# Kernel tuning notes

Measured on AMD Instinct MI355X. Metric: run time of the kernel, lower is better.

## Reference

```python
import jax, jax.numpy as jnp
import numpy as np

H, F, D, E, L = 8, 768, 128, 256, 13   # heads, feat_dim, compression_dim, embed_dim, nb_layer
B, T = 8, 1000
DCOR = D * (D - 1) // 2                # 8128, upper-triangle (offset=1) correlation features


def setup_inputs() -> dict:
    key = jax.random.key(0)
    ks = jax.random.split(key, 12)
    s = lambda k, shape, sc=0.02: jax.random.normal(k, shape, jnp.float32) * sc
    return {
        "x": jax.random.normal(ks[0], (B, F, T, L), jnp.float32),
        "weights_k": jnp.ones((H, L), jnp.float32),
        "weights_v": jnp.ones((H, L), jnp.float32),
        "q": jax.random.normal(ks[1], (H, D), jnp.float32),
        "Wk": s(ks[2], (H, D, F)), "bk": s(ks[3], (H, D)),
        "Wv": s(ks[4], (H, D, F)), "bv": s(ks[5], (H, D)),
        "Wproj": s(ks[6], (H, E, DCOR)), "bproj": s(ks[7], (H, E)),
        "WT": s(ks[8], (E, H * D)), "bT": s(ks[9], (E,)),
        "Wp": s(ks[10], (E, H * E)), "bp": s(ks[11], (E,)),
    }


def _norm_t(z):
    # normalize over the time axis; torch .var() is unbiased (ddof=1)
    mu = z.mean(axis=2, keepdims=True)
    sd = jnp.sqrt(z.var(axis=2, keepdims=True, ddof=1)) + 1e-9
    return (z - mu) / sd


def _forward(x, weights_k, weights_v, q, Wk, bk, Wv, bv, Wproj, bproj, WT, bT, Wp, bp):
    # x: [B, F, T, L]; per-head softmax-weighted layer sum -> [B, H, T, F]
    kw = jax.nn.softmax(weights_k, axis=-1)  # [H, L]
    vw = jax.nn.softmax(weights_v, axis=-1)
    k_raw = jnp.einsum('bftl,hl->bhtf', x, kw)
    v_raw = jnp.einsum('bftl,hl->bhtf', x, vw)
    # per-head compression linears -> [B, H, T, D]
    mh_k = jnp.einsum('bhtf,hdf->bhtd', k_raw, Wk) + bk[None, :, None, :]
    mh_v = jnp.einsum('bhtf,hdf->bhtd', v_raw, Wv) + bv[None, :, None, :]
    # single-query scaled-dot-product attention pooling per head
    scores = jnp.einsum('hd,bhtd->bht', q, mh_k) / jnp.sqrt(jnp.float32(D))
    attn = jax.nn.softmax(scores, axis=-1)
    o1 = jnp.einsum('bht,bhtd->bhd', attn, mh_v)           # [B, H, D]
    out_T = o1.reshape(B, H * D) @ WT.T + bT               # [B, E]
    # correlation branch (mh_q = mh_v): time-normalize, D x D correlation, triu(offset=1)
    k_n = _norm_t(mh_k)
    q_n = _norm_t(mh_v)
    corr = jnp.einsum('bhtk,bhtl->bhkl', k_n, q_n) / T     # [B, H, D, D]
    iu0, iu1 = np.triu_indices(D, k=1)
    mh_corr = corr[:, :, iu0, iu1]                         # [B, H, DCOR]
    outs = jnp.einsum('bhc,hec->bhe', mh_corr, Wproj) + bproj[None]
    out_F = outs.reshape(B, H * E) @ Wp.T + bp             # [B, E]
    return 0.5 * out_F + 0.5 * out_T


def reference(x, weights_k, weights_v, q, Wk, bk, Wv, bv, Wproj, bproj, WT, bT, Wp, bp):
    return _forward(x, weights_k, weights_v, q, Wk, bk, Wv, bv, Wproj, bproj, WT, bT, Wp, bp)
```

## Files before the change

### kernel.cpp

```cpp
#include <hip/hip_runtime.h>
#include <hip/hip_bf16.h>

#define Hn 8
#define Fn 768
#define Dn 128
#define En 256
#define Ln 13
#define Bn 8
#define Tn 1000
#define TPn 1024
#define NCOR 8128

typedef float f32x4 __attribute__((ext_vector_type(4)));
typedef __bf16 bf16x8 __attribute__((ext_vector_type(8)));
typedef unsigned short u16;

static __device__ __forceinline__ u16 f2bf(float f) {
  __hip_bfloat16 h = __float2bfloat16(f);
  return __builtin_bit_cast(u16, h);
}
static __device__ __forceinline__ float bf2f(u16 u) {
  return __bfloat162float(__builtin_bit_cast(__hip_bfloat16, u));
}

static __device__ __forceinline__ void gload_lds16(const u16* g, u16* lds_wave_base) {
  __builtin_amdgcn_global_load_lds(
      (const __attribute__((address_space(1))) unsigned int*)g,
      (__attribute__((address_space(3))) unsigned int*)lds_wave_base, 16, 0, 0);
}

__global__ __launch_bounds__(256) void k1_raw(
    const float* __restrict__ x,
    const float* __restrict__ wk, const float* __restrict__ wv,
    const float* __restrict__ Wk, const float* __restrict__ Wv,
    u16* __restrict__ kv_raw, u16* __restrict__ Wbf,
    float* __restrict__ s1, float* __restrict__ s2,
    int b0, int BG) {
  __shared__ float kvw[16 * Ln];
  __shared__ u16 res[16 * 32 * 34];
  int tid = threadIdx.x;
  if (tid < 16) {
    int kvi = tid >> 3, h = tid & 7;
    const float* w = (kvi ? wv : wk) + h * Ln;
    float m = -1e30f;
    for (int l = 0; l < Ln; ++l) m = fmaxf(m, w[l]);
    float e[Ln], s = 0.f;
    for (int l = 0; l < Ln; ++l) { e[l] = expf(w[l] - m); s += e[l]; }
    for (int l = 0; l < Ln; ++l) kvw[tid * Ln + l] = e[l] / s;
  }
  if (b0 == 0) {
    int nb = gridDim.x * gridDim.y * gridDim.z;
    int lin = blockIdx.x + gridDim.x * (blockIdx.y + gridDim.y * blockIdx.z);
    int n = 2 * Hn * Dn * Fn;
    for (int i = lin * 256 + tid; i < n; i += nb * 256) {
      float v = (i < Hn * Dn * Fn) ? Wk[i] : Wv[i - Hn * Dn * Fn];
      Wbf[i] = f2bf(v);
    }
    int ns = 2 * Bn * Hn * Dn;
    for (int i = lin * 256 + tid; i < ns; i += nb * 256) { s1[i] = 0.f; s2[i] = 0.f; }
  }
  int t0 = blockIdx.x * 32, f0 = blockIdx.y * 32;
  int b_l = blockIdx.z, b = b0 + b_l;
  int fl = tid & 31, tq = tid >> 5;
  int tbase = t0 + tq * 4;
  bool valid = (tbase < Tn);
  float4 xq[13];
  if (valid) {
    const float4* xp = (const float4*)(x + ((size_t)(b * Fn + f0 + fl) * Tn + tbase) * Ln);
#pragma unroll
    for (int i = 0; i < 13; ++i) xq[i] = xp[i];
  }
  __syncthreads();
  const float* xf = (const float*)xq;
  for (int o = 0; o < 16; ++o) {
    float a0 = 0.f, a1 = 0.f, a2 = 0.f, a3 = 0.f;
    if (valid) {
#pragma unroll
      for (int l = 0; l < Ln; ++l) {
        float w = kvw[o * Ln + l];
        a0 += xf[l] * w;
        a1 += xf[Ln + l] * w;
        a2 += xf[2 * Ln + l] * w;
        a3 += xf[3 * Ln + l] * w;
      }
    }
    int rb = o * 1088 + tq * 4 * 34 + fl;
    res[rb] = f2bf(a0);
    res[rb + 34] = f2bf(a1);
    res[rb + 68] = f2bf(a2);
    res[rb + 102] = f2bf(a3);
  }
  __syncthreads();
  int part = tid & 3;
#pragma unroll
  for (int it = 0; it < 8; ++it) {
    int r = (tid >> 2) + it * 64;
    int o = r >> 5, tl = r & 31;
    int kv = o >> 3, h = o & 7;
    const u16* src = res + o * 1088 + tl * 34 + part * 8;
    uint4 v;
    v.x = *(const unsigned*)(src + 0);
    v.y = *(const unsigned*)(src + 2);
    v.z = *(const unsigned*)(src + 4);
    v.w = *(const unsigned*)(src + 6);
    u16* dst = kv_raw + (((size_t)(kv * BG + b_l) * Hn + h) * TPn + t0 + tl) * Fn + f0 + part * 8;
    *reinterpret_cast<uint4*>(dst) = v;
  }
}

__global__ __launch_bounds__(256) void k2_gemm(
    const u16* __restrict__ kv_raw, const u16* __restrict__ Wbf,
    const float* __restrict__ bk, const float* __restrict__ bv,
    const float* __restrict__ qg,
    u16* __restrict__ mhT, float* __restrict__ s1buf, float* __restrict__ s2buf,
    float* __restrict__ scores, int b0, int BG) {
  __shared__ __align__(16) char ldsbuf[33280];
  __shared__ float qsh[Dn];
  u16* As0 = (u16*)ldsbuf;
  u16* Bs0 = (u16*)(ldsbuf + 8192);
  u16* As1 = (u16*)(ldsbuf + 16384);
  u16* Bs1 = (u16*)(ldsbuf + 24576);
  u16* Cst = (u16*)ldsbuf;
  int tid = threadIdx.x, lane = tid & 63, w = tid >> 6;
  int t0 = blockIdx.x * 128;
  int b_l = blockIdx.y / Hn, h = blockIdx.y % Hn, kv = blockIdx.z;
  int b = b0 + b_l;
  if (tid < Dn) qsh[tid] = qg[h * Dn + tid];
  const u16* Abase = kv_raw + ((size_t)(kv * BG + b_l) * Hn + h) * TPn * Fn + (size_t)t0 * Fn;
  const u16* Bbase = Wbf + ((size_t)(kv * Hn + h)) * Dn * Fn;
  f32x4 acc[4][4];
#pragma unroll
  for (int mi = 0; mi < 4; ++mi)
#pragma unroll
    for (int ni = 0; ni < 4; ++ni) acc[mi][ni] = (f32x4){0.f, 0.f, 0.f, 0.f};
  int wm = (w >> 1) * 64, wn = (w & 1) * 64;
  int lin0 = tid, lin1 = tid + 256;
  int row0 = lin0 >> 2, part0 = lin0 & 3;
  int row1 = lin1 >> 2, part1 = lin1 & 3;
  int wb0 = (w * 64) * 8, wb1 = (256 + w * 64) * 8;

  auto STAGE = [&](int f0, u16* Ad, u16* Bd) {
    gload_lds16(Abase + (size_t)row0 * Fn + f0 + part0 * 8, Ad + wb0);
    gload_lds16(Abase + (size_t)row1 * Fn + f0 + part1 * 8, Ad + wb1);
    gload_lds16(Bbase + (size_t)row0 * Fn + f0 + part0 * 8, Bd + wb0);
    gload_lds16(Bbase + (size_t)row1 * Fn + f0 + part1 * 8, Bd + wb1);
  };
  auto COMPUTE = [&](const u16* Ac, const u16* Bc) {
    bf16x8 af[4], bg[4];
#pragma unroll
    for (int mi = 0; mi < 4; ++mi)
      af[mi] = *(const bf16x8*)(Ac + (wm + mi * 16 + (lane & 15)) * 32 + (lane >> 4) * 8);
#pragma unroll
    for (int ni = 0; ni < 4; ++ni)
      bg[ni] = *(const bf16x8*)(Bc + (wn + ni * 16 + (lane & 15)) * 32 + (lane >> 4) * 8);
#pragma unroll
    for (int mi = 0; mi < 4; ++mi)
#pragma unroll
      for (int ni = 0; ni < 4; ++ni)
        acc[mi][ni] = __builtin_amdgcn_mfma_f32_16x16x32_bf16(af[mi], bg[ni], acc[mi][ni], 0, 0, 0);
  };

  STAGE(0, As0, Bs0);
  __syncthreads();
  for (int f0 = 0; f0 < Fn; f0 += 64) {
    if (f0 + 32 < Fn) STAGE(f0 + 32, As1, Bs1);
    COMPUTE(As0, Bs0);
    __syncthreads();
    if (f0 + 64 < Fn) STAGE(f0 + 64, As0, Bs0);
    COMPUTE(As1, Bs1);
    __syncthreads();
  }

  float bias[4];
  const float* bptr = (kv ? bv : bk) + h * Dn;
#pragma unroll
  for (int ni = 0; ni < 4; ++ni) bias[ni] = bptr[wn + ni * 16 + (lane & 15)];
#pragma unroll
  for (int mi = 0; mi < 4; ++mi)
#pragma unroll
    for (int ni = 0; ni < 4; ++ni)
#pragma unroll
      for (int r = 0; r < 4; ++r) {
        int row = wm + mi * 16 + (lane >> 4) * 4 + r;
        int col = wn + ni * 16 + (lane & 15);
        float v = acc[mi][ni][r] + bias[ni];
        if (t0 + row >= Tn) v = 0.f;
        Cst[row * 130 + col] = f2bf(v);
      }
  __syncthreads();
  int d = tid >> 1, half = tid & 1;
  u16* orow = mhT + (((size_t)(kv * Bn + b) * Hn + h) * Dn + d) * TPn + t0;
  float ssum = 0.f, ssq = 0.f;
#pragma unroll
  for (int j = 0; j < 8; ++j) {
    int tb = half * 64 + j * 8;
    u16 pk[8];
#pragma unroll
    for (int ii = 0; ii < 8; ++ii) {
      u16 ub = Cst[(tb + ii) * 130 + d];
      pk[ii] = ub;
      float vr = bf2f(ub);
      ssum += vr;
      ssq += vr * vr;
    }
    uint4 v4;
    v4.x = (unsigned)pk[0] | ((unsigned)pk[1] << 16);
    v4.y = (unsigned)pk[2] | ((unsigned)pk[3] << 16);
    v4.z = (unsigned)pk[4] | ((unsigned)pk[5] << 16);
    v4.w = (unsigned)pk[6] | ((unsigned)pk[7] << 16);
    *reinterpret_cast<uint4*>(orow + tb) = v4;
  }
  int sidx = ((kv * Bn + b) * Hn + h) * Dn + d;
  atomicAdd(&s1buf[sidx], ssum);
  atomicAdd(&s2buf[sidx], ssq);

  if (kv == 0) {
    int t = tid >> 1, hf = tid & 1;
    float s = 0.f;
    const u16* crow = Cst + t * 130 + hf * 64;
    const float* qh = qsh + hf * 64;
#pragma unroll
    for (int dd = 0; dd < 64; ++dd) s += qh[dd] * bf2f(crow[dd]);
    s += __shfl_xor(s, 1);
    if (hf == 0)
      scores[((size_t)b * Hn + h) * TPn + t0 + t] =
          (t0 + t < Tn) ? s * 0.088388347648318447f : -1e30f;
  }
}

__global__ __launch_bounds__(256) void k34(
    const u16* __restrict__ mhT, const float* __restrict__ scores,
    const float* __restrict__ s1buf, const float* __restrict__ s2buf,
    float* __restrict__ o1, float* __restrict__ corr) {
  __shared__ float sc[TPn];
  __shared__ float red[256];
  __shared__ __align__(16) u16 Kt0[1024], Vt0[4096], Kt1[1024], Vt1[4096];
  __shared__ float mkS[32], skS[32], mvS[128], svS[128];
  int tid = threadIdx.x;
  int lane = tid & 63, w = tid >> 6;
  if (blockIdx.x < 256) {
    int bh = blockIdx.x >> 2, dq = blockIdx.x & 3;
    int b = bh >> 3, h = bh & 7;
    const float* srow = scores + (size_t)bh * TPn;
    float4 z4 = *((const float4*)srow + tid);
    float z[4] = {z4.x, z4.y, z4.z, z4.w};
    float m = fmaxf(fmaxf(z[0], z[1]), fmaxf(z[2], z[3]));
#pragma unroll
    for (int off = 32; off; off >>= 1) m = fmaxf(m, __shfl_xor(m, off));
    if (lane == 0) red[w] = m;
    __syncthreads();
    m = fmaxf(fmaxf(red[0], red[1]), fmaxf(red[2], red[3]));
    float lsum = 0.f;
#pragma unroll
    for (int j = 0; j < 4; ++j) {
      float e = __expf(z[j] - m);
      sc[tid * 4 + j] = e;
      lsum += e;
    }
#pragma unroll
    for (int off = 32; off; off >>= 1) lsum += __shfl_xor(lsum, off);
    if (lane == 0) red[4 + w] = lsum;
    __syncthreads();
    float inv = 1.f / (red[4] + red[5] + red[6] + red[7]);
    int dl = tid & 31, slice = tid >> 5;
    int d = dq * 32 + dl;
    const u16* Vr = mhT + ((size_t)(1 * Bn + b) * Hn + h) * Dn * TPn + (size_t)d * TPn + slice * 128;
    const float* at = sc + slice * 128;
    float a = 0.f;
#pragma unroll
    for (int i = 0; i < 16; ++i) {
      bf16x8 vv = *(const bf16x8*)(Vr + i * 8);
#pragma unroll
      for (int j = 0; j < 8; ++j) a += at[i * 8 + j] * (float)vv[j];
    }
    a += __shfl_xor(a, 32);
    __syncthreads();
    if (lane < 32) red[w * 32 + dl] = a;
    __syncthreads();
    if (tid < 32)
      o1[((size_t)b * Hn + h) * Dn + dq * 32 + tid] =
          inv * (red[tid] + red[32 + tid] + red[64 + tid] + red[96 + tid]);
    return;
  }
  int id = blockIdx.x - 256;
  int bh = id & 63, rq = id >> 6;
  int b = bh >> 3, h = bh & 7;
  const u16* Kb = mhT + ((size_t)(0 * Bn + b) * Hn + h) * Dn * TPn + (size_t)(rq * 32) * TPn;
  const u16* Vb = mhT + ((size_t)(1 * Bn + b) * Hn + h) * Dn * TPn;
  if (tid < 32) {
    int dd = rq * 32 + tid;
    int sidx = ((0 * Bn + b) * Hn + h) * Dn + dd;
    float a1 = s1buf[sidx], a2 = s2buf[sidx];
    float mu = a1 / (float)Tn;
    float var = (a2 - a1 * a1 / (float)Tn) / (float)(Tn - 1);
    mkS[tid] = mu;
    skS[tid] = sqrtf(fmaxf(var, 0.f)) + 1e-9f;
  } else if (tid < 160) {
    int dd = tid - 32;
    int sidx = ((1 * Bn + b) * Hn + h) * Dn + dd;
    float a1 = s1buf[sidx], a2 = s2buf[sidx];
    float mu = a1 / (float)Tn;
    float var = (a2 - a1 * a1 / (float)Tn) / (float)(Tn - 1);
    mvS[dd] = mu;
    svS[dd] = sqrtf(fmaxf(var, 0.f)) + 1e-9f;
  }
  f32x4 acc[2][2];
#pragma unroll
  for (int mi = 0; mi < 2; ++mi)
#pragma unroll
    for (int ni = 0; ni < 2; ++ni) acc[mi][ni] = (f32x4){0.f, 0.f, 0.f, 0.f};
  int rowK = tid >> 2, partK = tid & 3;
  int wbK = (w * 64) * 8;
  int rowV0 = tid >> 2, partV0 = tid & 3;
  int rowV1 = (tid + 256) >> 2, partV1 = tid & 3;
  int wbV0 = (w * 64) * 8, wbV1 = (256 + w * 64) * 8;

  auto STAGE = [&](int t0, u16* Kd, u16* Vd) {
    if (w < 2)
      gload_lds16(Kb + (size_t)rowK * TPn + t0 + partK * 8, Kd + wbK);
    gload_lds16(Vb + (size_t)rowV0 * TPn + t0 + partV0 * 8, Vd + wbV0);
    gload_lds16(Vb + (size_t)rowV1 * TPn + t0 + partV1 * 8, Vd + wbV1);
  };
  auto COMPUTE = [&](const u16* Kc, const u16* Vc) {
    bf16x8 af[2], bg[2];
#pragma unroll
    for (int mi = 0; mi < 2; ++mi)
      af[mi] = *(const bf16x8*)(Kc + (mi * 16 + (lane & 15)) * 32 + (lane >> 4) * 8);
#pragma unroll
    for (int ni = 0; ni < 2; ++ni)
      bg[ni] = *(const bf16x8*)(Vc + (w * 32 + ni * 16 + (lane & 15)) * 32 + (lane >> 4) * 8);
#pragma unroll
    for (int mi = 0; mi < 2; ++mi)
#pragma unroll
      for (int ni = 0; ni < 2; ++ni)
        acc[mi][ni] = __builtin_amdgcn_mfma_f32_16x16x32_bf16(af[mi], bg[ni], acc[mi][ni], 0, 0, 0);
  };

  STAGE(0, Kt0, Vt0);
  __syncthreads();
  for (int s = 0; s < TPn; s += 64) {
    if (s + 32 < TPn) STAGE(s + 32, Kt1, Vt1);
    COMPUTE(Kt0, Vt0);
    __syncthreads();
    if (s + 64 < TPn) STAGE(s + 64, Kt0, Vt0);
    COMPUTE(Kt1, Vt1);
    __syncthreads();
  }
  const float invT = 1.f / (float)Tn;
#pragma unroll
  for (int mi = 0; mi < 2; ++mi)
#pragma unroll
    for (int ni = 0; ni < 2; ++ni)
#pragma unroll
      for (int r = 0; r < 4; ++r) {
        int ml = mi * 16 + (lane >> 4) * 4 + r;
        int nn = w * 32 + ni * 16 + (lane & 15);
        int mm = rq * 32 + ml;
        if (nn > mm) {
          float S = acc[mi][ni][r];
          float cv = (S - (float)Tn * mkS[ml] * mvS[nn]) * invT / (skS[ml] * svS[nn]);
          int cidx = mm * (2 * Dn - mm - 1) / 2 + (nn - mm - 1);
          corr[(size_t)bh * NCOR + cidx] = cv;
        }
      }
}

__global__ __launch_bounds__(256) void k5_proj(
    const float* __restrict__ corr, const float* __restrict__ Wproj,
    const float* __restrict__ bproj, float* __restrict__ outs) {
  __shared__ float red[8 * 256];
  int tid = threadIdx.x;
  int e = blockIdx.x, h = blockIdx.y;
  const float4* wp4 = (const float4*)(Wproj + ((size_t)h * En + e) * NCOR);
  float accs[8];
#pragma unroll
  for (int b = 0; b < 8; ++b) accs[b] = 0.f;
  for (int k = 0; k < 8; ++k) {
    int c4 = tid + k * 256;
    if (c4 < NCOR / 4) {
      float4 wv = wp4[c4];
#pragma unroll
      for (int b = 0; b < 8; ++b) {
        float4 cv = *((const float4*)(corr + ((size_t)b * Hn + h) * NCOR) + c4);
        accs[b] += wv.x * cv.x + wv.y * cv.y + wv.z * cv.z + wv.w * cv.w;
      }
    }
  }
#pragma unroll
  for (int b = 0; b < 8; ++b) red[b * 256 + tid] = accs[b];
  __syncthreads();
  for (int s = 128; s > 0; s >>= 1) {
    if (tid < s) {
#pragma unroll
      for (int b = 0; b < 8; ++b) red[b * 256 + tid] += red[b * 256 + tid + s];
    }
    __syncthreads();
  }
  if (tid < 8) outs[((size_t)tid * Hn + h) * En + e] = red[tid * 256] + bproj[h * En + e];
}

__global__ __launch_bounds__(256) void k5_final(
    const float* __restrict__ outs, const float* __restrict__ o1,
    const float* __restrict__ WT, const float* __restrict__ bT,
    const float* __restrict__ Wp, const float* __restrict__ bp,
    float* __restrict__ out) {
  __shared__ float os[2048];
  __shared__ float o1s[1024];
  __shared__ float redF[256], redT[256];
  int tid = threadIdx.x;
  int b = blockIdx.x >> 3, ic = blockIdx.x & 7;
  for (int i = tid; i < 2048; i += 256) os[i] = outs[(size_t)b * 2048 + i];
  for (int i = tid; i < 1024; i += 256) o1s[i] = o1[(size_t)b * 1024 + i];
  __syncthreads();
  int il = tid >> 3, slice = tid & 7;
  int i = ic * 32 + il;
  const float* wpr = Wp + (size_t)i * 2048;
  const float* wtr = WT + (size_t)i * 1024;
  float aF = 0.f, aT = 0.f;
  for (int kk = 0; kk < 256; ++kk) { int j = kk * 8 + slice; aF += os[j] * wpr[j]; }
  for (int kk = 0; kk < 128; ++kk) { int j = kk * 8 + slice; aT += o1s[j] * wtr[j]; }
  redF[tid] = aF; redT[tid] = aT;
  __syncthreads();
  for (int s = 4; s > 0; s >>= 1) {
    if (slice < s) { redF[tid] += redF[tid + s]; redT[tid] += redT[tid + s]; }
    __syncthreads();
  }
  if (slice == 0) {
    float oF = redF[tid] + bp[i];
    float oT = redT[tid] + bT[i];
    out[(size_t)b * En + i] = 0.5f * oF + 0.5f * oT;
  }
}

extern "C" void kernel_launch(void* const* d_in, const int* in_sizes, int n_in,
                              void* d_out, int out_size, void* d_ws, size_t ws_size,
                              hipStream_t stream) {
  const float* x     = (const float*)d_in[0];
  const float* wk    = (const float*)d_in[1];
  const float* wv    = (const float*)d_in[2];
  const float* q     = (const float*)d_in[3];
  const float* Wk    = (const float*)d_in[4];
  const float* bk    = (const float*)d_in[5];
  const float* Wv    = (const float*)d_in[6];
  const float* bv    = (const float*)d_in[7];
  const float* Wproj = (const float*)d_in[8];
  const float* bproj = (const float*)d_in[9];
  const float* WT    = (const float*)d_in[10];
  const float* bT    = (const float*)d_in[11];
  const float* Wp    = (const float*)d_in[12];
  const float* bp    = (const float*)d_in[13];
  float* out = (float*)d_out;

  char* ws = (char*)d_ws;
  size_t off = 0;
  auto alloc = [&](size_t bytes) { size_t p = off; off += (bytes + 255) & ~(size_t)255; return p; };
  u16*   Wbf    = (u16*)  (ws + alloc((size_t)2 * Hn * Dn * Fn * 2));
  u16*   mhT    = (u16*)  (ws + alloc((size_t)2 * Bn * Hn * Dn * TPn * 2));
  float* s1     = (float*)(ws + alloc((size_t)2 * Bn * Hn * Dn * 4));
  float* s2     = (float*)(ws + alloc((size_t)2 * Bn * Hn * Dn * 4));
  float* o1     = (float*)(ws + alloc((size_t)Bn * Hn * Dn * 4));
  float* corr   = (float*)(ws + alloc((size_t)Bn * Hn * NCOR * 4));
  float* outs   = (float*)(ws + alloc((size_t)Bn * Hn * En * 4));
  float* scores = (float*)(ws + alloc((size_t)Bn * Hn * TPn * 4));
  size_t fixed = off;
  size_t per_b = (size_t)2 * Hn * TPn * Fn * 2;
  int BG = 8;
  while (BG > 1 && fixed + (size_t)BG * per_b > ws_size) BG >>= 1;
  u16* kv_raw = (u16*)(ws + fixed);

  for (int b0 = 0; b0 < Bn; b0 += BG) {
    k1_raw<<<dim3(32, 24, BG), 256, 0, stream>>>(x, wk, wv, Wk, Wv, kv_raw, Wbf, s1, s2, b0, BG);
    k2_gemm<<<dim3(8, Hn * BG, 2), 256, 0, stream>>>(kv_raw, Wbf, bk, bv, q, mhT, s1, s2,
                                                     scores, b0, BG);
  }
  k34<<<512, 256, 0, stream>>>(mhT, scores, s1, s2, o1, corr);
  k5_proj<<<dim3(En, Hn), 256, 0, stream>>>(corr, Wproj, bproj, outs);
  k5_final<<<64, 256, 0, stream>>>(outs, o1, WT, bT, Wp, bp, out);
}
```

Before: 661.0 us.

## Retile correlation and projection kernels, reorder GEMM grid, use nontemporal x loads

The correlation kernel now has each block compute 64 K-rows instead of 32, which halves the number of correlation blocks and the re-reads of the V tiles. The projection kernel now computes 8 output features per block, so each loaded corr vector is reused across 8 Wproj rows, and the shared-memory tree reduction is replaced by wave shuffles. The k2 grid is reordered so batch-head varies fastest. The one-shot x reads use nontemporal loads. The trade-off is higher register pressure (64 accumulators in the projection kernel) and fewer blocks, which may lower occupancy.

```diff
diff --git a/kernel.cpp b/kernel.cpp
--- a/kernel.cpp
+++ b/kernel.cpp
@@ -64,11 +64,11 @@
   int fl = tid & 31, tq = tid >> 5;
   int tbase = t0 + tq * 4;
   bool valid = (tbase < Tn);
-  float4 xq[13];
+  f32x4 xq[13];
   if (valid) {
-    const float4* xp = (const float4*)(x + ((size_t)(b * Fn + f0 + fl) * Tn + tbase) * Ln);
-#pragma unroll
-    for (int i = 0; i < 13; ++i) xq[i] = xp[i];
+    const f32x4* xp = (const f32x4*)(x + ((size_t)(b * Fn + f0 + fl) * Tn + tbase) * Ln);
+#pragma unroll
+    for (int i = 0; i < 13; ++i) xq[i] = __builtin_nontemporal_load(xp + i);
   }
   __syncthreads();
   const float* xf = (const float*)xq;
@@ -122,8 +122,10 @@
   u16* Bs1 = (u16*)(ldsbuf + 24576);
   u16* Cst = (u16*)ldsbuf;
   int tid = threadIdx.x, lane = tid & 63, w = tid >> 6;
-  int t0 = blockIdx.x * 128;
-  int b_l = blockIdx.y / Hn, h = blockIdx.y % Hn, kv = blockIdx.z;
+  int bh_lin = blockIdx.x;
+  int b_l = bh_lin / Hn, h = bh_lin % Hn;
+  int t0 = blockIdx.y * 128;
+  int kv = blockIdx.z;
   int b = b0 + b_l;
   if (tid < Dn) qsh[tid] = qg[h * Dn + tid];
   const u16* Abase = kv_raw + ((size_t)(kv * BG + b_l) * Hn + h) * TPn * Fn + (size_t)t0 * Fn;
@@ -234,12 +236,13 @@
     float* __restrict__ o1, float* __restrict__ corr) {
   __shared__ float sc[TPn];
   __shared__ float red[256];
-  __shared__ __align__(16) u16 Kt0[1024], Vt0[4096], Kt1[1024], Vt1[4096];
-  __shared__ float mkS[32], skS[32], mvS[128], svS[128];
+  __shared__ __align__(16) u16 Kt0[4096 / 2], Vt0[4096], Kt1[4096 / 2], Vt1[4096];
+  __shared__ float mkS[64], skS[64], mvS[128], svS[128];
   int tid = threadIdx.x;
   int lane = tid & 63, w = tid >> 6;
-  if (blockIdx.x < 256) {
-    int bh = blockIdx.x >> 2, dq = blockIdx.x & 3;
+  if (blockIdx.x >= 128) {
+    int id = blockIdx.x - 128;
+    int bh = id >> 2, dq = id & 3;
     int b = bh >> 3, h = bh & 7;
     const float* srow = scores + (size_t)bh * TPn;
     float4 z4 = *((const float4*)srow + tid);
@@ -282,21 +285,21 @@
           inv * (red[tid] + red[32 + tid] + red[64 + tid] + red[96 + tid]);
     return;
   }
-  int id = blockIdx.x - 256;
-  int bh = id & 63, rq = id >> 6;
+  int id = blockIdx.x;
+  int bh = id & 63, rh = id >> 6;
   int b = bh >> 3, h = bh & 7;
-  const u16* Kb = mhT + ((size_t)(0 * Bn + b) * Hn + h) * Dn * TPn + (size_t)(rq * 32) * TPn;
+  const u16* Kb = mhT + ((size_t)(0 * Bn + b) * Hn + h) * Dn * TPn + (size_t)(rh * 64) * TPn;
   const u16* Vb = mhT + ((size_t)(1 * Bn + b) * Hn + h) * Dn * TPn;
-  if (tid < 32) {
-    int dd = rq * 32 + tid;
+  if (tid < 64) {
+    int dd = rh * 64 + tid;
     int sidx = ((0 * Bn + b) * Hn + h) * Dn + dd;
     float a1 = s1buf[sidx], a2 = s2buf[sidx];
     float mu = a1 / (float)Tn;
     float var = (a2 - a1 * a1 / (float)Tn) / (float)(Tn - 1);
     mkS[tid] = mu;
     skS[tid] = sqrtf(fmaxf(var, 0.f)) + 1e-9f;
-  } else if (tid < 160) {
-    int dd = tid - 32;
+  } else if (tid < 192) {
+    int dd = tid - 64;
     int sidx = ((1 * Bn + b) * Hn + h) * Dn + dd;
     float a1 = s1buf[sidx], a2 = s2buf[sidx];
     float mu = a1 / (float)Tn;
@@ -304,33 +307,31 @@
     mvS[dd] = mu;
     svS[dd] = sqrtf(fmaxf(var, 0.f)) + 1e-9f;
   }
-  f32x4 acc[2][2];
-#pragma unroll
-  for (int mi = 0; mi < 2; ++mi)
+  f32x4 acc[4][2];
+#pragma unroll
+  for (int mi = 0; mi < 4; ++mi)
 #pragma unroll
     for (int ni = 0; ni < 2; ++ni) acc[mi][ni] = (f32x4){0.f, 0.f, 0.f, 0.f};
-  int rowK = tid >> 2, partK = tid & 3;
-  int wbK = (w * 64) * 8;
-  int rowV0 = tid >> 2, partV0 = tid & 3;
-  int rowV1 = (tid + 256) >> 2, partV1 = tid & 3;
-  int wbV0 = (w * 64) * 8, wbV1 = (256 + w * 64) * 8;
+  int rowA = tid >> 2, partA = tid & 3;
+  int rowV1 = 64 + (tid >> 2);
+  int wbA = (w * 64) * 8;
+  int wbV1 = 2048 + (w * 64) * 8;
 
   auto STAGE = [&](int t0, u16* Kd, u16* Vd) {
-    if (w < 2)
-      gload_lds16(Kb + (size_t)rowK * TPn + t0 + partK * 8, Kd + wbK);
-    gload_lds16(Vb + (size_t)rowV0 * TPn + t0 + partV0 * 8, Vd + wbV0);
-    gload_lds16(Vb + (size_t)rowV1 * TPn + t0 + partV1 * 8, Vd + wbV1);
+    gload_lds16(Kb + (size_t)rowA * TPn + t0 + partA * 8, Kd + wbA);
+    gload_lds16(Vb + (size_t)rowA * TPn + t0 + partA * 8, Vd + wbA);
+    gload_lds16(Vb + (size_t)rowV1 * TPn + t0 + partA * 8, Vd + wbV1);
   };
   auto COMPUTE = [&](const u16* Kc, const u16* Vc) {
-    bf16x8 af[2], bg[2];
-#pragma unroll
-    for (int mi = 0; mi < 2; ++mi)
+    bf16x8 af[4], bg[2];
+#pragma unroll
+    for (int mi = 0; mi < 4; ++mi)
       af[mi] = *(const bf16x8*)(Kc + (mi * 16 + (lane & 15)) * 32 + (lane >> 4) * 8);
 #pragma unroll
     for (int ni = 0; ni < 2; ++ni)
       bg[ni] = *(const bf16x8*)(Vc + (w * 32 + ni * 16 + (lane & 15)) * 32 + (lane >> 4) * 8);
 #pragma unroll
-    for (int mi = 0; mi < 2; ++mi)
+    for (int mi = 0; mi < 4; ++mi)
 #pragma unroll
       for (int ni = 0; ni < 2; ++ni)
         acc[mi][ni] = __builtin_amdgcn_mfma_f32_16x16x32_bf16(af[mi], bg[ni], acc[mi][ni], 0, 0, 0);
@@ -348,14 +349,14 @@
   }
   const float invT = 1.f / (float)Tn;
 #pragma unroll
-  for (int mi = 0; mi < 2; ++mi)
+  for (int mi = 0; mi < 4; ++mi)
 #pragma unroll
     for (int ni = 0; ni < 2; ++ni)
 #pragma unroll
       for (int r = 0; r < 4; ++r) {
         int ml = mi * 16 + (lane >> 4) * 4 + r;
         int nn = w * 32 + ni * 16 + (lane & 15);
-        int mm = rq * 32 + ml;
+        int mm = rh * 64 + ml;
         if (nn > mm) {
           float S = acc[mi][ni][r];
           float cv = (S - (float)Tn * mkS[ml] * mvS[nn]) * invT / (skS[ml] * svS[nn]);
@@ -368,35 +369,44 @@
 __global__ __launch_bounds__(256) void k5_proj(
     const float* __restrict__ corr, const float* __restrict__ Wproj,
     const float* __restrict__ bproj, float* __restrict__ outs) {
-  __shared__ float red[8 * 256];
-  int tid = threadIdx.x;
-  int e = blockIdx.x, h = blockIdx.y;
-  const float4* wp4 = (const float4*)(Wproj + ((size_t)h * En + e) * NCOR);
-  float accs[8];
-#pragma unroll
-  for (int b = 0; b < 8; ++b) accs[b] = 0.f;
+  __shared__ float red[256];
+  int tid = threadIdx.x, lane = tid & 63, w = tid >> 6;
+  int h = blockIdx.x & 7, ec = blockIdx.x >> 3;
+  float acc[8][8];
+#pragma unroll
+  for (int ei = 0; ei < 8; ++ei)
+#pragma unroll
+    for (int b = 0; b < 8; ++b) acc[ei][b] = 0.f;
   for (int k = 0; k < 8; ++k) {
     int c4 = tid + k * 256;
     if (c4 < NCOR / 4) {
-      float4 wv = wp4[c4];
-#pragma unroll
-      for (int b = 0; b < 8; ++b) {
-        float4 cv = *((const float4*)(corr + ((size_t)b * Hn + h) * NCOR) + c4);
-        accs[b] += wv.x * cv.x + wv.y * cv.y + wv.z * cv.z + wv.w * cv.w;
+      float4 cv[8];
+#pragma unroll
+      for (int b = 0; b < 8; ++b)
+        cv[b] = *((const float4*)(corr + ((size_t)b * Hn + h) * NCOR) + c4);
+#pragma unroll
+      for (int ei = 0; ei < 8; ++ei) {
+        float4 wv = *((const float4*)(Wproj + ((size_t)h * En + ec * 8 + ei) * NCOR) + c4);
+#pragma unroll
+        for (int b = 0; b < 8; ++b)
+          acc[ei][b] += wv.x * cv[b].x + wv.y * cv[b].y + wv.z * cv[b].z + wv.w * cv[b].w;
       }
     }
   }
-#pragma unroll
-  for (int b = 0; b < 8; ++b) red[b * 256 + tid] = accs[b];
-  __syncthreads();
-  for (int s = 128; s > 0; s >>= 1) {
-    if (tid < s) {
-#pragma unroll
-      for (int b = 0; b < 8; ++b) red[b * 256 + tid] += red[b * 256 + tid + s];
-    }
-    __syncthreads();
-  }
-  if (tid < 8) outs[((size_t)tid * Hn + h) * En + e] = red[tid * 256] + bproj[h * En + e];
+  const float* af = &acc[0][0];
+#pragma unroll
+  for (int v = 0; v < 64; ++v) {
+    float s = af[v];
+#pragma unroll
+    for (int off = 32; off; off >>= 1) s += __shfl_xor(s, off);
+    if (lane == 0) red[w * 64 + v] = s;
+  }
+  __syncthreads();
+  if (tid < 64) {
+    int ei = tid >> 3, b = tid & 7;
+    float s = red[tid] + red[64 + tid] + red[128 + tid] + red[192 + tid];
+    outs[((size_t)b * Hn + h) * En + ec * 8 + ei] = s + bproj[h * En + ec * 8 + ei];
+  }
 }
 
 __global__ __launch_bounds__(256) void k5_final(
@@ -470,10 +480,10 @@
 
   for (int b0 = 0; b0 < Bn; b0 += BG) {
     k1_raw<<<dim3(32, 24, BG), 256, 0, stream>>>(x, wk, wv, Wk, Wv, kv_raw, Wbf, s1, s2, b0, BG);
-    k2_gemm<<<dim3(8, Hn * BG, 2), 256, 0, stream>>>(kv_raw, Wbf, bk, bv, q, mhT, s1, s2,
+    k2_gemm<<<dim3(Hn * BG, 8, 2), 256, 0, stream>>>(kv_raw, Wbf, bk, bv, q, mhT, s1, s2,
                                                      scores, b0, BG);
   }
-  k34<<<512, 256, 0, stream>>>(mhT, scores, s1, s2, o1, corr);
-  k5_proj<<<dim3(En, Hn), 256, 0, stream>>>(corr, Wproj, bproj, outs);
+  k34<<<384, 256, 0, stream>>>(mhT, scores, s1, s2, o1, corr);
+  k5_proj<<<256, 256, 0, stream>>>(corr, Wproj, bproj, outs);
   k5_final<<<64, 256, 0, stream>>>(outs, o1, WT, bT, Wp, bp, out);
 }
```

After: 752.0 us. 1.14x slower.
